# Kernel optimization log

Hardware: AMD Instinct MI355X
Metric: run time of the kernel (lower is better)

The kernel has to match this reference:

```python
import jax, jax.numpy as jnp
import numpy as np

B, N, DIM, H, D = 32, 151, 512, 8, 64


def _rel_pos(enc, cls, n, d):
    # enc: (b, n-1) float; cls: (1,1) scalar prepended per-row
    b = enc.shape[0]
    e = jnp.concatenate([jnp.broadcast_to(cls, (b, 1)), enc], axis=1)  # (b, n)
    i = jnp.arange(d)
    freq = jnp.power(10000.0, 2.0 * (i // 2).astype(jnp.float32) / d)  # (d,)
    pe = jnp.floor((e[:, :, None] * n) / freq)  # matches numpy '//' floor-div, (b,n,d)
    pe = jnp.where(i % 2 == 0, jnp.sin(pe), jnp.cos(pe))
    return pe[:, None, :, :] - pe[:, :, None, :]  # (b, n, n, d)


def setup_inputs() -> dict:
    key = jax.random.key(0)
    ks = jax.random.split(key, 6)
    x = jax.random.normal(ks[0], (B, N, DIM), jnp.float32)
    angle_enc = jax.random.uniform(ks[1], (B, N - 1), jnp.float32)
    W_qkv = jax.random.normal(ks[2], (DIM, 3 * H * D), jnp.float32) / np.sqrt(DIM)
    W_out = jax.random.normal(ks[3], (H * D, DIM), jnp.float32) / np.sqrt(H * D)
    b_out = jnp.zeros((DIM,), jnp.float32)
    cls_dist = jax.random.uniform(ks[4], (1, 1), jnp.float32)
    cls_angle = jax.random.uniform(ks[5], (1, 1), jnp.float32)
    return {"x": x, "angle_enc": angle_enc, "W_qkv": W_qkv, "W_out": W_out,
            "b_out": b_out, "cls_dist": cls_dist, "cls_angle": cls_angle}


def reference(x, angle_enc, W_qkv, W_out, b_out, cls_dist, cls_angle):
    b, n, _ = x.shape
    qkv = x @ W_qkv  # (b, n, 3*H*D)
    q, k, v = jnp.split(qkv, 3, axis=-1)
    sh = lambda t: t.reshape(b, n, H, D).transpose(0, 2, 1, 3)  # (b,H,n,D)
    q, k, v = sh(q), sh(k), sh(v)

    attn1 = jnp.einsum('bhnd,bhmd->bhnm', q, k)
    r_k2 = _rel_pos(angle_enc, cls_dist, n, D)        # (b,n,n,D)
    attn2 = jnp.einsum('bhnd,bnmd->bhnm', q, r_k2)
    attn = jax.nn.softmax((attn1 + attn2) * (D ** -0.5), axis=-1)

    w1 = jnp.einsum('bhnm,bhmd->bhnd', attn, v)
    r_v2 = _rel_pos(angle_enc, cls_angle, n, D)       # (b,n,n,D)
    w2 = jnp.einsum('bhnm,bnmd->bhnd', attn, r_v2)

    out = (w1 + w2).transpose(0, 2, 1, 3).reshape(b, n, H * D)
    return out @ W_out + b_out
```

## Files before the change

### kernel.cpp

```cpp
#include <hip/hip_runtime.h>
#include <hip/hip_bf16.h>
#include <math.h>

#define B_ 32
#define N_ 151
#define DIM_ 512
#define H_ 8
#define D_ 64
#define M_ (B_*N_)
#define NPAD 160

typedef short bf16x8 __attribute__((ext_vector_type(8)));
typedef float f32x4  __attribute__((ext_vector_type(4)));

static __device__ __forceinline__ short f2bf(float f) {
  union { __hip_bfloat16 h; short s; } u;
  u.h = __float2bfloat16(f);
  return u.s;
}
static __device__ __forceinline__ float bf2f(short s) {
  union { short s; __hip_bfloat16 h; } u;
  u.s = s;
  return __bfloat162float(u.h);
}
static __device__ __forceinline__ void split_bf(float v, short& hi, short& lo) {
  hi = f2bf(v);
  lo = f2bf(v - bf2f(hi));
}
static __device__ __forceinline__ void gload16(const void* g, void* l) {
  __builtin_amdgcn_global_load_lds(
      (const __attribute__((address_space(1))) unsigned int*)(uintptr_t)g,
      (__attribute__((address_space(3))) unsigned int*)(unsigned int)(uintptr_t)l,
      16, 0, 0);
}

__global__ void pe_kernel(const float* __restrict__ angle_enc,
                          const float* __restrict__ cls_dist,
                          const float* __restrict__ cls_angle,
                          float* __restrict__ pe_k, float* __restrict__ pe_v) {
  int idx = blockIdx.x * 256 + threadIdx.x;
  if (idx >= M_ * 64) return;
  int bn = idx >> 6, d = idx & 63;
  int b = bn / N_, n = bn - b * N_;
  float ek = (n == 0) ? cls_dist[0]  : angle_enc[b*(N_-1) + (n-1)];
  float ev = (n == 0) ? cls_angle[0] : angle_enc[b*(N_-1) + (n-1)];
  float freq_f = (float)pow(10000.0, (double)(2*(d >> 1)) / 64.0);
  double freq = (double)freq_f;
  float pk = (float)floor(((double)ek * 151.0) / freq);
  float pv = (float)floor(((double)ev * 151.0) / freq);
  pe_k[idx] = (d & 1) ? cosf(pk) : sinf(pk);
  pe_v[idx] = (d & 1) ? cosf(pv) : sinf(pv);
}

__global__ void cvt_bf16_kernel(const float* __restrict__ in, short* __restrict__ out, int n4) {
  int i = blockIdx.x * 256 + threadIdx.x;
  if (i < n4) {
    float4 v = ((const float4*)in)[i];
    short4 o;
    o.x = f2bf(v.x); o.y = f2bf(v.y); o.z = f2bf(v.z); o.w = f2bf(v.w);
    ((short4*)out)[i] = o;
  }
}

__global__ void transpose_bf16_kernel(const float* __restrict__ in, short* __restrict__ out,
                                      int R, int C) {
  __shared__ float tile[32][33];
  int tc = blockIdx.x * 32;
  int tr = blockIdx.y * 32;
  int lx = threadIdx.x & 31, ly = threadIdx.x >> 5;
  #pragma unroll
  for (int dy = 0; dy < 32; dy += 8)
    tile[ly + dy][lx] = in[(tr + ly + dy) * C + tc + lx];
  __syncthreads();
  #pragma unroll
  for (int dy = 0; dy < 32; dy += 8)
    out[(tc + ly + dy) * R + tr + lx] = f2bf(tile[lx][ly + dy]);
}

template<int EPI, int BM, int BN_, int WM, int WN>
__global__ __launch_bounds__(256, 2) void gemm_kernel(
    const short* __restrict__ A, const short* __restrict__ Bt,
    const float* __restrict__ pe_k, const float* __restrict__ pe_v,
    short* __restrict__ Qh, short* __restrict__ Ql,
    short* __restrict__ Kh, short* __restrict__ Vb,
    const float* __restrict__ bias, float* __restrict__ Out)
{
  constexpr int MI = BM / (WM * 16);
  constexpr int NI = BN_ / (WN * 16);
  constexpr int NT = DIM_ / 32;
  __shared__ short Ash[2][BM][32];
  __shared__ short Bsh[2][BN_][32];

  const int m0 = blockIdx.x * BM;
  const int n0 = blockIdx.y * BN_;
  const int t = threadIdx.x;
  const int wave = t >> 6, lane = t & 63;
  const int fr = lane & 15, fq = lane >> 4, fo = fq * 8;
  const int wr = wave / WN, wc = wave % WN;
  const int lrow = lane >> 2, lcol = (lane & 3) * 8;

  const f32x4 zero = {0.f, 0.f, 0.f, 0.f};
  f32x4 acc[MI][NI];
  #pragma unroll
  for (int i = 0; i < MI; i++)
    #pragma unroll
    for (int j = 0; j < NI; j++) acc[i][j] = zero;

  auto stage = [&](int buf, int k0) {
    #pragma unroll
    for (int c = 0; c < BM/16; c += 4) {
      int cc = c + wave;
      gload16(A + (long)(m0 + cc*16 + lrow) * DIM_ + k0 + lcol,
              &Ash[buf][0][0] + cc * 512);
    }
    #pragma unroll
    for (int c = 0; c < BN_/16; c += 4) {
      int cc = c + wave;
      gload16(Bt + (long)(n0 + cc*16 + lrow) * DIM_ + k0 + lcol,
              &Bsh[buf][0][0] + cc * 512);
    }
  };

  stage(0, 0);
  asm volatile("s_waitcnt vmcnt(0)" ::: "memory");
  __syncthreads();

  int cur = 0;
  for (int it = 0; it < NT; ++it) {
    if (it + 1 < NT) stage(cur ^ 1, (it + 1) * 32);

    bf16x8 af[MI], bf[NI];
    #pragma unroll
    for (int mi = 0; mi < MI; mi++)
      af[mi] = *(const bf16x8*)(&Ash[cur][wr * (BM/WM) + mi*16 + fr][fo]);
    #pragma unroll
    for (int ni = 0; ni < NI; ni++)
      bf[ni] = *(const bf16x8*)(&Bsh[cur][wc * (BN_/WN) + ni*16 + fr][fo]);
    #pragma unroll
    for (int mi = 0; mi < MI; mi++)
      #pragma unroll
      for (int ni = 0; ni < NI; ni++)
        acc[mi][ni] = __builtin_amdgcn_mfma_f32_16x16x32_bf16(af[mi], bf[ni], acc[mi][ni], 0, 0, 0);

    asm volatile("s_waitcnt vmcnt(0)" ::: "memory");
    __syncthreads();
    cur ^= 1;
  }

  #pragma unroll
  for (int mi = 0; mi < MI; mi++) {
    #pragma unroll
    for (int ni = 0; ni < NI; ni++) {
      #pragma unroll
      for (int r = 0; r < 4; r++) {
        int gm = m0 + wr * (BM/WM) + mi*16 + fq*4 + r;
        int gn = n0 + wc * (BN_/WN) + ni*16 + fr;
        if (gm >= M_) continue;
        float val = acc[mi][ni][r];
        if (EPI == 0) {
          int b = gm / N_, n = gm - b * N_;
          int sect = gn >> 9;
          int h = (gn >> 6) & 7;
          int d = gn & 63;
          int qi = ((b*H_ + h)*N_ + n)*64 + d;
          if (sect == 0) {
            short hi, lo; split_bf(val, hi, lo);
            Qh[qi] = hi; Ql[qi] = lo;
          } else if (sect == 1) {
            Kh[qi] = f2bf(val + pe_k[gm*64 + d]);
          } else {
            Vb[qi] = f2bf(val + pe_v[gm*64 + d]);
          }
        } else {
          Out[(long)gm*DIM_ + gn] = val + bias[gn];
        }
      }
    }
  }
}

__global__ __launch_bounds__(256, 2) void attn_kernel(
    const short* __restrict__ Qh, const short* __restrict__ Ql,
    const short* __restrict__ Kh,
    const short* __restrict__ Vb, const float* __restrict__ pe_v,
    short* __restrict__ Wh)
{
  __shared__ short Ksh[NPAD][72];
  __shared__ short Vt[64][NPAD + 8];
  __shared__ short Ps[4][16][NPAD + 8];

  const int bh = blockIdx.x;
  const int b = bh >> 3, h = bh & 7;
  const int t = threadIdx.x;
  const int wave = t >> 6, lane = t & 63;
  const int fr = lane & 15, fq = lane >> 4, fo = fq * 8;
  const int base = bh * (N_ * 64);

  {
    const int seg = t & 7, r0 = t >> 3;
    for (int r = r0; r < NPAD; r += 32) {
      bf16x8 kh = {0,0,0,0,0,0,0,0}, vv = {0,0,0,0,0,0,0,0};
      if (r < N_) {
        kh = *(const bf16x8*)(Kh + base + r*64 + seg*8);
        vv = *(const bf16x8*)(Vb + base + r*64 + seg*8);
      }
      *(bf16x8*)(&Ksh[r][seg*8]) = kh;
      #pragma unroll
      for (int j = 0; j < 8; j++) Vt[seg*8 + j][r] = vv[j];
    }
  }
  __syncthreads();

  const int s = blockIdx.y * 4 + wave;
  if (s < 10) {
    const int q0 = s * 16;
    const f32x4 zero = {0.f, 0.f, 0.f, 0.f};

    bf16x8 aq0h = {0,0,0,0,0,0,0,0}, aq1h = {0,0,0,0,0,0,0,0};
    bf16x8 aq0l = {0,0,0,0,0,0,0,0}, aq1l = {0,0,0,0,0,0,0,0};
    if (q0 + fr < N_) {
      const short* qrh = Qh + base + (q0 + fr) * 64;
      const short* qrl = Ql + base + (q0 + fr) * 64;
      aq0h = *(const bf16x8*)(qrh + fo);
      aq1h = *(const bf16x8*)(qrh + 32 + fo);
      aq0l = *(const bf16x8*)(qrl + fo);
      aq1l = *(const bf16x8*)(qrl + 32 + fo);
    }
    f32x4 sf[10];
    #pragma unroll
    for (int kt = 0; kt < 10; kt++) {
      bf16x8 bh0 = *(const bf16x8*)(&Ksh[kt*16 + fr][fo]);
      bf16x8 bh1 = *(const bf16x8*)(&Ksh[kt*16 + fr][32 + fo]);
      f32x4 s0 = __builtin_amdgcn_mfma_f32_16x16x32_bf16(aq0l, bh0, zero, 0, 0, 0);
      s0 = __builtin_amdgcn_mfma_f32_16x16x32_bf16(aq0h, bh0, s0, 0, 0, 0);
      s0 = __builtin_amdgcn_mfma_f32_16x16x32_bf16(aq1l, bh1, s0, 0, 0, 0);
      sf[kt] = __builtin_amdgcn_mfma_f32_16x16x32_bf16(aq1h, bh1, s0, 0, 0, 0);
    }
    #pragma unroll
    for (int kt = 0; kt < 10; kt++) {
      int col = kt*16 + fr;
      #pragma unroll
      for (int r = 0; r < 4; r++) {
        float v = sf[kt][r] * 0.125f;
        sf[kt][r] = (col < N_) ? v : -1e30f;
      }
    }
    float mx[4], sum[4];
    #pragma unroll
    for (int r = 0; r < 4; r++) {
      float m = sf[0][r];
      #pragma unroll
      for (int kt = 1; kt < 10; kt++) m = fmaxf(m, sf[kt][r]);
      #pragma unroll
      for (int off = 1; off < 16; off <<= 1) m = fmaxf(m, __shfl_xor(m, off));
      mx[r] = m;
    }
    #pragma unroll
    for (int kt = 0; kt < 10; kt++)
      #pragma unroll
      for (int r = 0; r < 4; r++)
        sf[kt][r] = exp2f((sf[kt][r] - mx[r]) * 1.4426950408889634f);
    #pragma unroll
    for (int r = 0; r < 4; r++) {
      float sm = 0.f;
      #pragma unroll
      for (int kt = 0; kt < 10; kt++) sm += sf[kt][r];
      #pragma unroll
      for (int off = 1; off < 16; off <<= 1) sm += __shfl_xor(sm, off);
      sum[r] = sm;
    }
    #pragma unroll
    for (int kt = 0; kt < 10; kt++)
      #pragma unroll
      for (int r = 0; r < 4; r++)
        Ps[wave][fq*4 + r][kt*16 + fr] = f2bf(sf[kt][r]);
    f32x4 o[4] = {zero, zero, zero, zero};
    #pragma unroll
    for (int kc = 0; kc < 5; kc++) {
      bf16x8 pa = *(const bf16x8*)(&Ps[wave][fr][kc*32 + fo]);
      #pragma unroll
      for (int nb = 0; nb < 4; nb++) {
        bf16x8 bv = *(const bf16x8*)(&Vt[nb*16 + fr][kc*32 + fo]);
        o[nb] = __builtin_amdgcn_mfma_f32_16x16x32_bf16(pa, bv, o[nb], 0, 0, 0);
      }
    }
    float inv[4];
    #pragma unroll
    for (int r = 0; r < 4; r++) inv[r] = 1.0f / sum[r];
    #pragma unroll
    for (int nb = 0; nb < 4; nb++) {
      #pragma unroll
      for (int r = 0; r < 4; r++) {
        int n = q0 + fq*4 + r;
        if (n < N_) {
          int d = nb*16 + fr;
          float val = o[nb][r] * inv[r] - pe_v[(b*N_ + n)*64 + d];
          Wh[(b*N_ + n)*DIM_ + h*64 + d] = f2bf(val);
        }
      }
    }
  }
}

extern "C" void kernel_launch(void* const* d_in, const int* in_sizes, int n_in,
                              void* d_out, int out_size, void* d_ws, size_t ws_size,
                              hipStream_t stream) {
  const float* x         = (const float*)d_in[0];
  const float* angle_enc = (const float*)d_in[1];
  const float* W_qkv     = (const float*)d_in[2];
  const float* W_out     = (const float*)d_in[3];
  const float* b_out     = (const float*)d_in[4];
  const float* cls_dist  = (const float*)d_in[5];
  const float* cls_angle = (const float*)d_in[6];

  char* ws = (char*)d_ws;
  size_t off = 0;
  auto carve = [&](size_t bytes) { size_t o = off; off += (bytes + 255) & ~(size_t)255; return o; };
  const size_t MD2 = (size_t)M_ * DIM_ * 2;

  float* pe_k = (float*)(ws + carve((size_t)M_ * 64 * 4));
  float* pe_v = (float*)(ws + carve((size_t)M_ * 64 * 4));
  short* xb   = (short*)(ws + carve(MD2));
  short* wqT  = (short*)(ws + carve((size_t)1536 * 512 * 2));
  short* woT  = (short*)(ws + carve((size_t)512 * 512 * 2));
  short* Qhb  = (short*)(ws + carve(MD2));
  short* Qlb  = (short*)(ws + carve(MD2));
  short* Khb  = (short*)(ws + carve(MD2));
  short* Vb   = (short*)(ws + carve(MD2));
  short* Wh   = xb;

  pe_kernel<<<(M_*64 + 255)/256, 256, 0, stream>>>(angle_enc, cls_dist, cls_angle, pe_k, pe_v);

  int n4 = (M_ * DIM_) / 4;
  cvt_bf16_kernel<<<(n4 + 255) / 256, 256, 0, stream>>>(x, xb, n4);
  transpose_bf16_kernel<<<dim3(1536/32, 512/32), 256, 0, stream>>>(W_qkv, wqT, 512, 1536);
  transpose_bf16_kernel<<<dim3(512/32, 512/32), 256, 0, stream>>>(W_out, woT, 512, 512);

  gemm_kernel<0, 64, 128, 1, 4><<<dim3((M_ + 63)/64, 1536/128), 256, 0, stream>>>(
      xb, wqT, pe_k, pe_v, Qhb, Qlb, Khb, Vb, nullptr, nullptr);

  attn_kernel<<<dim3(B_ * H_, 3), 256, 0, stream>>>(Qhb, Qlb, Khb, Vb, pe_v, Wh);

  gemm_kernel<1, 64, 64, 2, 2><<<dim3((M_ + 63)/64, DIM_/64), 256, 0, stream>>>(
      Wh, woT, nullptr, nullptr, nullptr, nullptr, nullptr, nullptr,
      b_out, (float*)d_out);
}
```

Before: 143.4 us.

## Fuse prep kernels, drop Q hi/lo split, pre-transpose V, widen GEMM K-tile

```diff
diff --git a/kernel.cpp b/kernel.cpp
--- a/kernel.cpp
+++ b/kernel.cpp
@@ -18,15 +18,6 @@
   u.h = __float2bfloat16(f);
   return u.s;
 }
-static __device__ __forceinline__ float bf2f(short s) {
-  union { short s; __hip_bfloat16 h; } u;
-  u.s = s;
-  return __bfloat162float(u.h);
-}
-static __device__ __forceinline__ void split_bf(float v, short& hi, short& lo) {
-  hi = f2bf(v);
-  lo = f2bf(v - bf2f(hi));
-}
 static __device__ __forceinline__ void gload16(const void* g, void* l) {
   __builtin_amdgcn_global_load_lds(
       (const __attribute__((address_space(1))) unsigned int*)(uintptr_t)g,
@@ -34,70 +25,78 @@
       16, 0, 0);
 }
 
-__global__ void pe_kernel(const float* __restrict__ angle_enc,
-                          const float* __restrict__ cls_dist,
-                          const float* __restrict__ cls_angle,
-                          float* __restrict__ pe_k, float* __restrict__ pe_v) {
-  int idx = blockIdx.x * 256 + threadIdx.x;
-  if (idx >= M_ * 64) return;
-  int bn = idx >> 6, d = idx & 63;
-  int b = bn / N_, n = bn - b * N_;
-  float ek = (n == 0) ? cls_dist[0]  : angle_enc[b*(N_-1) + (n-1)];
-  float ev = (n == 0) ? cls_angle[0] : angle_enc[b*(N_-1) + (n-1)];
-  float freq_f = (float)pow(10000.0, (double)(2*(d >> 1)) / 64.0);
-  double freq = (double)freq_f;
-  float pk = (float)floor(((double)ek * 151.0) / freq);
-  float pv = (float)floor(((double)ev * 151.0) / freq);
-  pe_k[idx] = (d & 1) ? cosf(pk) : sinf(pk);
-  pe_v[idx] = (d & 1) ? cosf(pv) : sinf(pv);
-}
-
-__global__ void cvt_bf16_kernel(const float* __restrict__ in, short* __restrict__ out, int n4) {
-  int i = blockIdx.x * 256 + threadIdx.x;
-  if (i < n4) {
-    float4 v = ((const float4*)in)[i];
+__global__ __launch_bounds__(256) void prep_kernel(
+    const float* __restrict__ x, const float* __restrict__ W_qkv,
+    const float* __restrict__ W_out, const float* __restrict__ angle_enc,
+    const float* __restrict__ cls_dist, const float* __restrict__ cls_angle,
+    short* __restrict__ xb, short* __restrict__ wqT, short* __restrict__ woT,
+    float* __restrict__ pe_k, float* __restrict__ pe_v)
+{
+  __shared__ float smf[32*33];
+  const int bx = blockIdx.x;
+  const int t = threadIdx.x;
+  const int lx = t & 31, ly = t >> 5;
+
+  {
+    const float* in; short* out; int R, C, tc, tr;
+    if (bx < 768) { in = W_qkv; out = wqT; R = 512; C = 1536; tc = (bx % 48) * 32; tr = (bx / 48) * 32; }
+    else          { in = W_out; out = woT; R = 512; C = 512;  tc = ((bx - 768) % 16) * 32; tr = ((bx - 768) / 16) * 32; }
+    float (*tile)[33] = (float(*)[33])smf;
+    #pragma unroll
+    for (int dy = 0; dy < 32; dy += 8)
+      tile[ly + dy][lx] = in[(tr + ly + dy) * C + tc + lx];
+    __syncthreads();
+    #pragma unroll
+    for (int dy = 0; dy < 32; dy += 8)
+      out[(tc + ly + dy) * R + tr + lx] = f2bf(tile[lx][ly + dy]);
+  }
+  __syncthreads();
+
+  if (t < 32) smf[t] = (float)pow(10000.0, (double)t / 32.0);
+  __syncthreads();
+
+  for (int idx = bx * 256 + t; idx < M_ * 64; idx += 1024 * 256) {
+    int bn = idx >> 6, d = idx & 63;
+    int b = bn / N_, n = bn - b * N_;
+    float ek = (n == 0) ? cls_dist[0]  : angle_enc[b*(N_-1) + (n-1)];
+    float ev = (n == 0) ? cls_angle[0] : angle_enc[b*(N_-1) + (n-1)];
+    double freq = (double)smf[(d >> 1)];
+    float pk = (float)floor(((double)ek * 151.0) / freq);
+    float pv = (float)floor(((double)ev * 151.0) / freq);
+    pe_k[idx] = (d & 1) ? cosf(pk) : sinf(pk);
+    pe_v[idx] = (d & 1) ? cosf(pv) : sinf(pv);
+  }
+
+  const int n4 = (M_ * DIM_) / 4;
+  for (int i = bx * 256 + t; i < n4; i += 1024 * 256) {
+    float4 v = ((const float4*)x)[i];
     short4 o;
     o.x = f2bf(v.x); o.y = f2bf(v.y); o.z = f2bf(v.z); o.w = f2bf(v.w);
-    ((short4*)out)[i] = o;
-  }
-}
-
-__global__ void transpose_bf16_kernel(const float* __restrict__ in, short* __restrict__ out,
-                                      int R, int C) {
-  __shared__ float tile[32][33];
-  int tc = blockIdx.x * 32;
-  int tr = blockIdx.y * 32;
-  int lx = threadIdx.x & 31, ly = threadIdx.x >> 5;
-  #pragma unroll
-  for (int dy = 0; dy < 32; dy += 8)
-    tile[ly + dy][lx] = in[(tr + ly + dy) * C + tc + lx];
-  __syncthreads();
-  #pragma unroll
-  for (int dy = 0; dy < 32; dy += 8)
-    out[(tc + ly + dy) * R + tr + lx] = f2bf(tile[lx][ly + dy]);
+    ((short4*)xb)[i] = o;
+  }
 }
 
 template<int EPI, int BM, int BN_, int WM, int WN>
-__global__ __launch_bounds__(256, 2) void gemm_kernel(
+__global__ __launch_bounds__(256, 3) void gemm_kernel(
     const short* __restrict__ A, const short* __restrict__ Bt,
     const float* __restrict__ pe_k, const float* __restrict__ pe_v,
-    short* __restrict__ Qh, short* __restrict__ Ql,
-    short* __restrict__ Kh, short* __restrict__ Vb,
+    short* __restrict__ Qb, short* __restrict__ Kh, short* __restrict__ Vtg,
     const float* __restrict__ bias, float* __restrict__ Out)
 {
   constexpr int MI = BM / (WM * 16);
   constexpr int NI = BN_ / (WN * 16);
-  constexpr int NT = DIM_ / 32;
-  __shared__ short Ash[2][BM][32];
-  __shared__ short Bsh[2][BN_][32];
+  constexpr int NT = DIM_ / 64;
+  __shared__ short Ash[2][BM][64];
+  __shared__ short Bsh[2][BN_][64];
 
   const int m0 = blockIdx.x * BM;
   const int n0 = blockIdx.y * BN_;
   const int t = threadIdx.x;
   const int wave = t >> 6, lane = t & 63;
-  const int fr = lane & 15, fq = lane >> 4, fo = fq * 8;
+  const int fr = lane & 15, fq = lane >> 4;
   const int wr = wave / WN, wc = wave % WN;
-  const int lrow = lane >> 2, lcol = (lane & 3) * 8;
+  const int srow = lane >> 3;
+  const int scol = ((lane & 7) ^ srow) << 3;
 
   const f32x4 zero = {0.f, 0.f, 0.f, 0.f};
   f32x4 acc[MI][NI];
@@ -108,17 +107,11 @@
 
   auto stage = [&](int buf, int k0) {
     #pragma unroll
-    for (int c = 0; c < BM/16; c += 4) {
-      int cc = c + wave;
-      gload16(A + (long)(m0 + cc*16 + lrow) * DIM_ + k0 + lcol,
-              &Ash[buf][0][0] + cc * 512);
-    }
-    #pragma unroll
-    for (int c = 0; c < BN_/16; c += 4) {
-      int cc = c + wave;
-      gload16(Bt + (long)(n0 + cc*16 + lrow) * DIM_ + k0 + lcol,
-              &Bsh[buf][0][0] + cc * 512);
-    }
+    for (int c = wave; c < BM/8; c += 4)
+      gload16(A + (long)(m0 + c*8 + srow) * DIM_ + k0 + scol, &Ash[buf][c*8][0]);
+    #pragma unroll
+    for (int c = wave; c < BN_/8; c += 4)
+      gload16(Bt + (long)(n0 + c*8 + srow) * DIM_ + k0 + scol, &Bsh[buf][c*8][0]);
   };
 
   stage(0, 0);
@@ -127,26 +120,32 @@
 
   int cur = 0;
   for (int it = 0; it < NT; ++it) {
-    if (it + 1 < NT) stage(cur ^ 1, (it + 1) * 32);
-
-    bf16x8 af[MI], bf[NI];
-    #pragma unroll
-    for (int mi = 0; mi < MI; mi++)
-      af[mi] = *(const bf16x8*)(&Ash[cur][wr * (BM/WM) + mi*16 + fr][fo]);
-    #pragma unroll
-    for (int ni = 0; ni < NI; ni++)
-      bf[ni] = *(const bf16x8*)(&Bsh[cur][wc * (BN_/WN) + ni*16 + fr][fo]);
-    #pragma unroll
-    for (int mi = 0; mi < MI; mi++)
+    if (it + 1 < NT) stage(cur ^ 1, (it + 1) * 64);
+
+    #pragma unroll
+    for (int kk = 0; kk < 2; kk++) {
+      const int rc = (kk*32 + fq*8) ^ ((fr & 7) << 3);
+      bf16x8 af[MI], bf[NI];
+      #pragma unroll
+      for (int mi = 0; mi < MI; mi++)
+        af[mi] = *(const bf16x8*)(&Ash[cur][wr * (BM/WM) + mi*16 + fr][rc]);
       #pragma unroll
       for (int ni = 0; ni < NI; ni++)
-        acc[mi][ni] = __builtin_amdgcn_mfma_f32_16x16x32_bf16(af[mi], bf[ni], acc[mi][ni], 0, 0, 0);
+        bf[ni] = *(const bf16x8*)(&Bsh[cur][wc * (BN_/WN) + ni*16 + fr][rc]);
+      #pragma unroll
+      for (int mi = 0; mi < MI; mi++)
+        #pragma unroll
+        for (int ni = 0; ni < NI; ni++)
+          acc[mi][ni] = __builtin_amdgcn_mfma_f32_16x16x32_bf16(af[mi], bf[ni], acc[mi][ni], 0, 0, 0);
+    }
 
     asm volatile("s_waitcnt vmcnt(0)" ::: "memory");
     __syncthreads();
     cur ^= 1;
   }
 
+  const int fo = fq * 8;
+  (void)fo;
   #pragma unroll
   for (int mi = 0; mi < MI; mi++) {
     #pragma unroll
@@ -162,14 +161,13 @@
           int sect = gn >> 9;
           int h = (gn >> 6) & 7;
           int d = gn & 63;
-          int qi = ((b*H_ + h)*N_ + n)*64 + d;
+          int bh = b*H_ + h;
           if (sect == 0) {
-            short hi, lo; split_bf(val, hi, lo);
-            Qh[qi] = hi; Ql[qi] = lo;
+            Qb[(bh*N_ + n)*64 + d] = f2bf(val);
           } else if (sect == 1) {
-            Kh[qi] = f2bf(val + pe_k[gm*64 + d]);
+            Kh[(bh*N_ + n)*64 + d] = f2bf(val + pe_k[gm*64 + d]);
           } else {
-            Vb[qi] = f2bf(val + pe_v[gm*64 + d]);
+            Vtg[((long)bh*64 + d)*160 + n] = f2bf(val + pe_v[gm*64 + d]);
           }
         } else {
           Out[(long)gm*DIM_ + gn] = val + bias[gn];
@@ -180,9 +178,8 @@
 }
 
 __global__ __launch_bounds__(256, 2) void attn_kernel(
-    const short* __restrict__ Qh, const short* __restrict__ Ql,
-    const short* __restrict__ Kh,
-    const short* __restrict__ Vb, const float* __restrict__ pe_v,
+    const short* __restrict__ Qb, const short* __restrict__ Kh,
+    const short* __restrict__ Vtg, const float* __restrict__ pe_v,
     short* __restrict__ Wh)
 {
   __shared__ short Ksh[NPAD][72];
@@ -199,14 +196,16 @@
   {
     const int seg = t & 7, r0 = t >> 3;
     for (int r = r0; r < NPAD; r += 32) {
-      bf16x8 kh = {0,0,0,0,0,0,0,0}, vv = {0,0,0,0,0,0,0,0};
-      if (r < N_) {
-        kh = *(const bf16x8*)(Kh + base + r*64 + seg*8);
-        vv = *(const bf16x8*)(Vb + base + r*64 + seg*8);
-      }
+      bf16x8 kh = {0,0,0,0,0,0,0,0};
+      if (r < N_) kh = *(const bf16x8*)(Kh + base + r*64 + seg*8);
       *(bf16x8*)(&Ksh[r][seg*8]) = kh;
-      #pragma unroll
-      for (int j = 0; j < 8; j++) Vt[seg*8 + j][r] = vv[j];
+    }
+    const int vrow = t >> 2;
+    const long vbase = ((long)bh * 64 + vrow) * 160;
+    #pragma unroll
+    for (int c = 0; c < 5; c++) {
+      int col = (t & 3) * 8 + c * 32;
+      *(bf16x8*)(&Vt[vrow][col]) = *(const bf16x8*)(Vtg + vbase + col);
     }
   }
   __syncthreads();
@@ -216,25 +215,19 @@
     const int q0 = s * 16;
     const f32x4 zero = {0.f, 0.f, 0.f, 0.f};
 
-    bf16x8 aq0h = {0,0,0,0,0,0,0,0}, aq1h = {0,0,0,0,0,0,0,0};
-    bf16x8 aq0l = {0,0,0,0,0,0,0,0}, aq1l = {0,0,0,0,0,0,0,0};
+    bf16x8 aq0 = {0,0,0,0,0,0,0,0}, aq1 = {0,0,0,0,0,0,0,0};
     if (q0 + fr < N_) {
-      const short* qrh = Qh + base + (q0 + fr) * 64;
-      const short* qrl = Ql + base + (q0 + fr) * 64;
-      aq0h = *(const bf16x8*)(qrh + fo);
-      aq1h = *(const bf16x8*)(qrh + 32 + fo);
-      aq0l = *(const bf16x8*)(qrl + fo);
-      aq1l = *(const bf16x8*)(qrl + 32 + fo);
+      const short* qr = Qb + base + (q0 + fr) * 64;
+      aq0 = *(const bf16x8*)(qr + fo);
+      aq1 = *(const bf16x8*)(qr + 32 + fo);
     }
     f32x4 sf[10];
     #pragma unroll
     for (int kt = 0; kt < 10; kt++) {
       bf16x8 bh0 = *(const bf16x8*)(&Ksh[kt*16 + fr][fo]);
       bf16x8 bh1 = *(const bf16x8*)(&Ksh[kt*16 + fr][32 + fo]);
-      f32x4 s0 = __builtin_amdgcn_mfma_f32_16x16x32_bf16(aq0l, bh0, zero, 0, 0, 0);
-      s0 = __builtin_amdgcn_mfma_f32_16x16x32_bf16(aq0h, bh0, s0, 0, 0, 0);
-      s0 = __builtin_amdgcn_mfma_f32_16x16x32_bf16(aq1l, bh1, s0, 0, 0, 0);
-      sf[kt] = __builtin_amdgcn_mfma_f32_16x16x32_bf16(aq1h, bh1, s0, 0, 0, 0);
+      f32x4 s0 = __builtin_amdgcn_mfma_f32_16x16x32_bf16(aq0, bh0, zero, 0, 0, 0);
+      sf[kt]   = __builtin_amdgcn_mfma_f32_16x16x32_bf16(aq1, bh1, s0, 0, 0, 0);
     }
     #pragma unroll
     for (int kt = 0; kt < 10; kt++) {
@@ -323,25 +316,20 @@
   short* xb   = (short*)(ws + carve(MD2));
   short* wqT  = (short*)(ws + carve((size_t)1536 * 512 * 2));
   short* woT  = (short*)(ws + carve((size_t)512 * 512 * 2));
-  short* Qhb  = (short*)(ws + carve(MD2));
-  short* Qlb  = (short*)(ws + carve(MD2));
+  short* Qb   = (short*)(ws + carve(MD2));
   short* Khb  = (short*)(ws + carve(MD2));
-  short* Vb   = (short*)(ws + carve(MD2));
+  short* Vtg  = (short*)(ws + carve((size_t)B_ * H_ * 64 * 160 * 2));
   short* Wh   = xb;
 
-  pe_kernel<<<(M_*64 + 255)/256, 256, 0, stream>>>(angle_enc, cls_dist, cls_angle, pe_k, pe_v);
-
-  int n4 = (M_ * DIM_) / 4;
-  cvt_bf16_kernel<<<(n4 + 255) / 256, 256, 0, stream>>>(x, xb, n4);
-  transpose_bf16_kernel<<<dim3(1536/32, 512/32), 256, 0, stream>>>(W_qkv, wqT, 512, 1536);
-  transpose_bf16_kernel<<<dim3(512/32, 512/32), 256, 0, stream>>>(W_out, woT, 512, 512);
+  prep_kernel<<<1024, 256, 0, stream>>>(x, W_qkv, W_out, angle_enc, cls_dist, cls_angle,
+                                        xb, wqT, woT, pe_k, pe_v);
 
   gemm_kernel<0, 64, 128, 1, 4><<<dim3((M_ + 63)/64, 1536/128), 256, 0, stream>>>(
-      xb, wqT, pe_k, pe_v, Qhb, Qlb, Khb, Vb, nullptr, nullptr);
-
-  attn_kernel<<<dim3(B_ * H_, 3), 256, 0, stream>>>(Qhb, Qlb, Khb, Vb, pe_v, Wh);
+      xb, wqT, pe_k, pe_v, Qb, Khb, Vtg, nullptr, nullptr);
+
+  attn_kernel<<<dim3(B_ * H_, 3), 256, 0, stream>>>(Qb, Khb, Vtg, pe_v, Wh);
 
   gemm_kernel<1, 64, 64, 2, 2><<<dim3((M_ + 63)/64, DIM_/64), 256, 0, stream>>>(
-      Wh, woT, nullptr, nullptr, nullptr, nullptr, nullptr, nullptr,
+      Wh, woT, nullptr, nullptr, nullptr, nullptr, nullptr,
       b_out, (float*)d_out);
 }
```

Result: faster. 135.4 us (-5.6%).
